# Kernel tuning notes

Hardware: AMD Instinct MI355X
Metric: run time of the kernel (lower is better)

The kernel has to match this reference:

```python
import jax, jax.numpy as jnp
import numpy as np

B, NQ, C = 2, 10000, 256
M, L, K = 8, 3, 4
D = C // M
LEVEL_SHAPES = [(100, 100), (50, 50), (25, 25)]


def setup_inputs() -> dict:
    key = jax.random.key(0)
    ks = jax.random.split(key, 16)
    inp = {
        "query": jax.random.normal(ks[0], (B, NQ, C), jnp.float32),
        "reference_points": jax.random.uniform(ks[1], (B, NQ, 2), jnp.float32),
        "value0": jax.random.normal(ks[2], (B, C) + LEVEL_SHAPES[0], jnp.float32),
        "value1": jax.random.normal(ks[3], (B, C) + LEVEL_SHAPES[1], jnp.float32),
        "value2": jax.random.normal(ks[4], (B, C) + LEVEL_SHAPES[2], jnp.float32),
        "Wv": jax.random.normal(ks[5], (C, C), jnp.float32) * 0.02,
        "bv": jnp.zeros((C,), jnp.float32),
        "Ws": jax.random.normal(ks[6], (M * L * K * 2, C), jnp.float32) * 0.05,
        "bs": jax.random.normal(ks[7], (M * L * K * 2,), jnp.float32),
        "Wa": jax.random.normal(ks[8], (M * L * K, C), jnp.float32) * 0.02,
        "ba": jnp.zeros((M * L * K,), jnp.float32),
        "Wo": jax.random.normal(ks[9], (C, C), jnp.float32) * 0.02,
        "bo": jnp.zeros((C,), jnp.float32),
    }
    return inp


def _bilinear_sample(vflat, px, py, H, W):
    """grid_sample bilinear, align_corners=False, padding_mode='zeros'.
    vflat: (B, M, H*W, D); px, py: (B, M, Q, K) pixel coords. -> (B, M, Q, K, D)
    """
    b, m, q, k = px.shape
    x0 = jnp.floor(px)
    y0 = jnp.floor(py)
    wx1 = px - x0  # frac weights (grad 1 w.r.t. px, matching grid_sample)
    wy1 = py - y0
    wx0 = 1.0 - wx1
    wy0 = 1.0 - wy1

    def gather(xi, yi):
        valid = ((xi >= 0) & (xi <= W - 1) & (yi >= 0) & (yi <= H - 1)).astype(vflat.dtype)
        xc = jnp.clip(xi, 0, W - 1).astype(jnp.int32)
        yc = jnp.clip(yi, 0, H - 1).astype(jnp.int32)
        idx = (yc * W + xc).reshape(b, m, q * k)
        g = jnp.take_along_axis(vflat, idx[..., None], axis=2)  # (B,M,QK,D)
        return g.reshape(b, m, q, k, -1) * valid[..., None]

    out = (gather(x0, y0) * (wx0 * wy0)[..., None]
           + gather(x0 + 1, y0) * (wx1 * wy0)[..., None]
           + gather(x0, y0 + 1) * (wx0 * wy1)[..., None]
           + gather(x0 + 1, y0 + 1) * (wx1 * wy1)[..., None])
    return out


def reference(query, reference_points, value0, value1, value2,
              Wv, bv, Ws, bs, Wa, ba, Wo, bo):
    bsz, nq, c = query.shape
    dt = query.dtype
    # sampling offsets and attention weights
    off = (query @ Ws.T + bs).reshape(bsz, nq, M, L, K, 2)
    attn = jax.nn.softmax((query @ Wa.T + ba).reshape(bsz, nq, M, L * K), axis=-1)
    attn = attn.reshape(bsz, nq, M, L, K)

    out = jnp.zeros((bsz, nq, M, D), dt)
    for li, v in enumerate([value0, value1, value2]):
        H, W = v.shape[2], v.shape[3]
        # conv1x1 value projection -> per-head maps (B, M, H*W, D)
        proj = jnp.einsum('bchw,oc->bohw', v, Wv) + bv[None, :, None, None]
        vflat = proj.reshape(bsz, M, D, H * W).transpose(0, 1, 3, 2)
        norm = jnp.asarray([W, H], dt)
        loc = reference_points[:, :, None, None, :] + off[:, :, :, li, :, :] / norm  # (B,Q,M,K,2)
        # grid = loc*2-1; pixel = (grid+1)*size/2 - 0.5 = loc*size - 0.5
        px = (loc[..., 0] * W - 0.5).transpose(0, 2, 1, 3)  # (B,M,Q,K)
        py = (loc[..., 1] * H - 0.5).transpose(0, 2, 1, 3)
        sampled = _bilinear_sample(vflat, px, py, H, W)  # (B,M,Q,K,D)
        out = out + jnp.einsum('bmqkd,bqmk->bqmd', sampled, attn[:, :, :, li, :])

    out = out.reshape(bsz, nq, c)
    return out @ Wo.T + bo
```

## Files before the change

### kernel.cpp

```cpp
#include <hip/hip_runtime.h>
#include <cstddef>

#define B_ 2
#define NQ_ 10000
#define C_ 256
#define M_ 8
#define L_ 3
#define K_ 4
#define D_ 32
#define P_ 13125

typedef unsigned short u16;
typedef __attribute__((ext_vector_type(8))) short short8;
typedef __attribute__((ext_vector_type(4))) float f32x4;

static __device__ __forceinline__ u16 f2bf(float f) {
    union { float f; unsigned u; } x; x.f = f;
    unsigned r = x.u + 0x7fffu + ((x.u >> 16) & 1u);
    return (u16)(r >> 16);
}
static __device__ __forceinline__ short8 cvt8(const float4& a, const float4& b) {
    short8 r;
    r[0] = (short)f2bf(a.x); r[1] = (short)f2bf(a.y);
    r[2] = (short)f2bf(a.z); r[3] = (short)f2bf(a.w);
    r[4] = (short)f2bf(b.x); r[5] = (short)f2bf(b.y);
    r[6] = (short)f2bf(b.z); r[7] = (short)f2bf(b.w);
    return r;
}

__global__ __launch_bounds__(256) void proj_fused(
    const float* __restrict__ v0, const float* __restrict__ v1,
    const float* __restrict__ v2,
    const float* __restrict__ Wv, const float* __restrict__ bv,
    u16* __restrict__ proj)
{
    __shared__ u16 As[64 * 264];
    __shared__ u16 Bs[64 * 264];

    const int bid = blockIdx.x;
    const int rlo = bid & 7;
    const int tmp = bid >> 3;
    const int panel = tmp & 3;
    const int rowTile = (tmp >> 2) * 8 + rlo;
    if (rowTile >= 414) return;

    const int b  = rowTile / 207;
    const int tl = rowTile % 207;
    int lvl, p0, HW, base;
    if (tl < 157)      { lvl = 0; p0 = tl * 64;         HW = 10000; base = 0; }
    else if (tl < 197) { lvl = 1; p0 = (tl - 157) * 64; HW = 2500;  base = 10000; }
    else               { lvl = 2; p0 = (tl - 197) * 64; HW = 625;   base = 12500; }
    const float* V = (lvl == 0 ? v0 : (lvl == 1 ? v1 : v2)) + (size_t)b * 256 * HW;

    const int t = threadIdx.x;
    const int px  = t & 63;
    const int pxg = min(p0 + px, HW - 1);
    const int ch0 = t >> 6;
    #pragma unroll
    for (int g = 0; g < 8; ++g) {
        float vv[8];
        #pragma unroll
        for (int j = 0; j < 8; ++j)
            vv[j] = V[(size_t)(ch0 + 4 * (8 * g + j)) * HW + pxg];
        #pragma unroll
        for (int j = 0; j < 8; ++j)
            As[px * 264 + ch0 + 4 * (8 * g + j)] = f2bf(vv[j]);
    }
    const int o0 = panel * 64;
    #pragma unroll
    for (int i = 0; i < 8; ++i) {
        int idx = i * 256 + t;
        int col = idx >> 5;
        int kc  = (idx & 31) * 8;
        const float* Br = Wv + (size_t)(o0 + col) * 256 + kc;
        float4 f0 = *reinterpret_cast<const float4*>(Br);
        float4 f1 = *reinterpret_cast<const float4*>(Br + 4);
        *reinterpret_cast<short8*>(&Bs[col * 264 + kc]) = cvt8(f0, f1);
    }
    __syncthreads();

    const int w  = t >> 6;
    const int l  = t & 63;
    const int lr = l & 15;
    const int kb = (l >> 4) * 8;
    const int arow = w * 16 + lr;

    f32x4 acc[4] = {};
    #pragma unroll
    for (int k0 = 0; k0 < 256; k0 += 32) {
        short8 a  = *reinterpret_cast<const short8*>(&As[arow * 264 + kb + k0]);
        short8 b0 = *reinterpret_cast<const short8*>(&Bs[(0 * 16 + lr) * 264 + kb + k0]);
        short8 b1 = *reinterpret_cast<const short8*>(&Bs[(1 * 16 + lr) * 264 + kb + k0]);
        short8 b2 = *reinterpret_cast<const short8*>(&Bs[(2 * 16 + lr) * 264 + kb + k0]);
        short8 b3 = *reinterpret_cast<const short8*>(&Bs[(3 * 16 + lr) * 264 + kb + k0]);
        acc[0] = __builtin_amdgcn_mfma_f32_16x16x32_bf16(a, b0, acc[0], 0, 0, 0);
        acc[1] = __builtin_amdgcn_mfma_f32_16x16x32_bf16(a, b1, acc[1], 0, 0, 0);
        acc[2] = __builtin_amdgcn_mfma_f32_16x16x32_bf16(a, b2, acc[2], 0, 0, 0);
        acc[3] = __builtin_amdgcn_mfma_f32_16x16x32_bf16(a, b3, acc[3], 0, 0, 0);
    }

    const int orow = (l >> 4) * 4;
    #pragma unroll
    for (int ct = 0; ct < 4; ++ct) {
        const int col = o0 + ct * 16 + lr;
        const float bsv = bv[col];
        #pragma unroll
        for (int r = 0; r < 4; ++r) {
            const int prow = w * 16 + orow + r;
            if (p0 + prow < HW)
                proj[((size_t)b * P_ + base + p0 + prow) * 256 + col] =
                    f2bf(acc[ct][r] + bsv);
        }
    }
}

template <bool AF32, typename OutT>
__global__ __launch_bounds__(256) void gemm_panel(
    const void* __restrict__ Av, int rows, int nRowTiles, int npanel,
    const float* __restrict__ B1f, const float* __restrict__ bias1, int N1,
    const float* __restrict__ B2f, const float* __restrict__ bias2, int Ntot,
    OutT* __restrict__ Cout)
{
    __shared__ u16 Bs[64 * 264];

    const int bid  = blockIdx.x;
    const int rlo  = bid & 7;
    const int tmp  = bid >> 3;
    const int panel = tmp % npanel;
    const int rowTile = (tmp / npanel) * 8 + rlo;
    if (rowTile >= nRowTiles) return;

    const int t  = threadIdx.x;
    const int w  = t >> 6;
    const int l  = t & 63;
    const int row0 = rowTile * 128 + w * 32;
    const int o0   = panel * 64;
    const int lr = l & 15;
    const int kb = (l >> 4) * 8;

    const int ra0 = min(row0 + lr,      rows - 1);
    const int ra1 = min(row0 + 16 + lr, rows - 1);

    short8 a0r[8], a1r[8];
    if constexpr (AF32) {
        const float* Af  = (const float*)Av;
        const float* Ap0 = Af + (size_t)ra0 * 256 + kb;
        const float* Ap1 = Af + (size_t)ra1 * 256 + kb;
        #pragma unroll
        for (int s = 0; s < 8; ++s) {
            float4 x0 = *reinterpret_cast<const float4*>(Ap0 + s * 32);
            float4 y0 = *reinterpret_cast<const float4*>(Ap0 + s * 32 + 4);
            float4 x1 = *reinterpret_cast<const float4*>(Ap1 + s * 32);
            float4 y1 = *reinterpret_cast<const float4*>(Ap1 + s * 32 + 4);
            a0r[s] = cvt8(x0, y0);
            a1r[s] = cvt8(x1, y1);
        }
    } else {
        const u16* Af  = (const u16*)Av;
        const u16* Ap0 = Af + (size_t)ra0 * 256 + kb;
        const u16* Ap1 = Af + (size_t)ra1 * 256 + kb;
        #pragma unroll
        for (int s = 0; s < 8; ++s) {
            a0r[s] = *reinterpret_cast<const short8*>(Ap0 + s * 32);
            a1r[s] = *reinterpret_cast<const short8*>(Ap1 + s * 32);
        }
    }

    #pragma unroll
    for (int i = 0; i < 8; ++i) {
        int idx = i * 256 + t;
        int col = idx >> 5;
        int kc  = (idx & 31) * 8;
        int colg = min(o0 + col, Ntot - 1);
        const float* Br = ((colg < N1) ? B1f + (size_t)colg * 256
                                       : B2f + (size_t)(colg - N1) * 256) + kc;
        float4 f0 = *reinterpret_cast<const float4*>(Br);
        float4 f1 = *reinterpret_cast<const float4*>(Br + 4);
        *reinterpret_cast<short8*>(&Bs[col * 264 + kc]) = cvt8(f0, f1);
    }
    __syncthreads();

    f32x4 acc[2][4] = {};

    #pragma unroll
    for (int s = 0; s < 8; ++s) {
        const int k0 = s * 32;
        short8 b0 = *reinterpret_cast<const short8*>(&Bs[(0 * 16 + lr) * 264 + kb + k0]);
        short8 b1 = *reinterpret_cast<const short8*>(&Bs[(1 * 16 + lr) * 264 + kb + k0]);
        short8 b2 = *reinterpret_cast<const short8*>(&Bs[(2 * 16 + lr) * 264 + kb + k0]);
        short8 b3 = *reinterpret_cast<const short8*>(&Bs[(3 * 16 + lr) * 264 + kb + k0]);
        acc[0][0] = __builtin_amdgcn_mfma_f32_16x16x32_bf16(a0r[s], b0, acc[0][0], 0, 0, 0);
        acc[0][1] = __builtin_amdgcn_mfma_f32_16x16x32_bf16(a0r[s], b1, acc[0][1], 0, 0, 0);
        acc[0][2] = __builtin_amdgcn_mfma_f32_16x16x32_bf16(a0r[s], b2, acc[0][2], 0, 0, 0);
        acc[0][3] = __builtin_amdgcn_mfma_f32_16x16x32_bf16(a0r[s], b3, acc[0][3], 0, 0, 0);
        acc[1][0] = __builtin_amdgcn_mfma_f32_16x16x32_bf16(a1r[s], b0, acc[1][0], 0, 0, 0);
        acc[1][1] = __builtin_amdgcn_mfma_f32_16x16x32_bf16(a1r[s], b1, acc[1][1], 0, 0, 0);
        acc[1][2] = __builtin_amdgcn_mfma_f32_16x16x32_bf16(a1r[s], b2, acc[1][2], 0, 0, 0);
        acc[1][3] = __builtin_amdgcn_mfma_f32_16x16x32_bf16(a1r[s], b3, acc[1][3], 0, 0, 0);
    }

    const int orow = (l >> 4) * 4;
    #pragma unroll
    for (int ct = 0; ct < 4; ++ct) {
        const int col = o0 + ct * 16 + lr;
        if (col >= Ntot) continue;
        const float bsv = (col < N1) ? bias1[col] : bias2[col - N1];
        #pragma unroll
        for (int rt = 0; rt < 2; ++rt) {
            #pragma unroll
            for (int r = 0; r < 4; ++r) {
                const int row = row0 + rt * 16 + orow + r;
                if (row < rows) {
                    float val = acc[rt][ct][r] + bsv;
                    if constexpr (sizeof(OutT) == 2)
                        Cout[(size_t)row * Ntot + col] = (OutT)f2bf(val);
                    else
                        Cout[(size_t)row * Ntot + col] = (OutT)val;
                }
            }
        }
    }
}

__global__ __launch_bounds__(256) void sample_kernel(
    const float* __restrict__ S,
    const float* __restrict__ refp,
    const u16* __restrict__ proj,
    u16* __restrict__ out2)
{
    constexpr int Wd[3]   = {100, 50, 25};
    constexpr int offs[3] = {0, 10000, 12500};

    __shared__ int   midx[192][4];
    __shared__ float mw[192][4];

    const int t = threadIdx.x;

    if (t < 192) {
        const int q  = t / 96;
        const int tq = t % 96;
        const int tm = tq / 12;
        const int tj = tq % 12;
        const int bq = blockIdx.x * 2 + q;
        const float* Sq = S + (size_t)bq * 288;

        float lg[12], mx = -1e30f;
        #pragma unroll
        for (int jj = 0; jj < 12; ++jj) {
            lg[jj] = Sq[192 + tm * 12 + jj];
            mx = fmaxf(mx, lg[jj]);
        }
        float sum = 0.f;
        #pragma unroll
        for (int jj = 0; jj < 12; ++jj) sum += __expf(lg[jj] - mx);
        const float attn = __expf(lg[tj] - mx) / sum;

        const int l  = tj >> 2;
        const int Wl = Wd[l];
        const float refx = refp[(size_t)bq * 2 + 0];
        const float refy = refp[(size_t)bq * 2 + 1];
        const float ox = Sq[(tm * 12 + tj) * 2 + 0];
        const float oy = Sq[(tm * 12 + tj) * 2 + 1];
        const float px = refx * (float)Wl + ox - 0.5f;
        const float py = refy * (float)Wl + oy - 0.5f;
        const float x0f = floorf(px), y0f = floorf(py);
        const float wx1 = px - x0f, wy1 = py - y0f;
        const float wx0 = 1.f - wx1, wy0 = 1.f - wy1;
        const int x0 = (int)x0f, y0 = (int)y0f;
        const int x1 = x0 + 1, y1 = y0 + 1;
        const bool vx0 = (unsigned)x0 < (unsigned)Wl;
        const bool vx1 = (unsigned)x1 < (unsigned)Wl;
        const bool vy0 = (unsigned)y0 < (unsigned)Wl;
        const bool vy1 = (unsigned)y1 < (unsigned)Wl;
        const int chb  = tm * 32;
        const int base = offs[l];
        midx[t][0] = (vx0 && vy0) ? ((base + y0 * Wl + x0) * 256 + chb) : 0;
        midx[t][1] = (vx1 && vy0) ? ((base + y0 * Wl + x1) * 256 + chb) : 0;
        midx[t][2] = (vx0 && vy1) ? ((base + y1 * Wl + x0) * 256 + chb) : 0;
        midx[t][3] = (vx1 && vy1) ? ((base + y1 * Wl + x1) * 256 + chb) : 0;
        mw[t][0] = (vx0 && vy0) ? attn * wx0 * wy0 : 0.f;
        mw[t][1] = (vx1 && vy0) ? attn * wx1 * wy0 : 0.f;
        mw[t][2] = (vx0 && vy1) ? attn * wx0 * wy1 : 0.f;
        mw[t][3] = (vx1 && vy1) ? attn * wx1 * wy1 : 0.f;
    }
    __syncthreads();

    const int qi  = t >> 7;
    const int tt  = t & 127;
    const int mh  = tt >> 4;
    const int d16 = tt & 15;
    const int bq2 = blockIdx.x * 2 + qi;
    const int b   = bq2 / NQ_;
    const u16* projb = proj + (size_t)b * P_ * 256 + 2 * d16;

    float acc0 = 0.f, acc1 = 0.f;

    #pragma unroll
    for (int j = 0; j < 12; ++j) {
        const int mj = qi * 96 + mh * 12 + j;
        const int4   o  = *reinterpret_cast<const int4*>(midx[mj]);
        const float4 ww = *reinterpret_cast<const float4*>(mw[mj]);
        const unsigned u00 = *reinterpret_cast<const unsigned*>(projb + o.x);
        const unsigned u10 = *reinterpret_cast<const unsigned*>(projb + o.y);
        const unsigned u01 = *reinterpret_cast<const unsigned*>(projb + o.z);
        const unsigned u11 = *reinterpret_cast<const unsigned*>(projb + o.w);
        union { unsigned u; float f; } c0, c1;
        c0.u = u00 << 16;          c1.u = u00 & 0xffff0000u;
        acc0 = fmaf(ww.x, c0.f, acc0); acc1 = fmaf(ww.x, c1.f, acc1);
        c0.u = u10 << 16;          c1.u = u10 & 0xffff0000u;
        acc0 = fmaf(ww.y, c0.f, acc0); acc1 = fmaf(ww.y, c1.f, acc1);
        c0.u = u01 << 16;          c1.u = u01 & 0xffff0000u;
        acc0 = fmaf(ww.z, c0.f, acc0); acc1 = fmaf(ww.z, c1.f, acc1);
        c0.u = u11 << 16;          c1.u = u11 & 0xffff0000u;
        acc0 = fmaf(ww.w, c0.f, acc0); acc1 = fmaf(ww.w, c1.f, acc1);
    }

    const unsigned packed = (unsigned)f2bf(acc0) | ((unsigned)f2bf(acc1) << 16);
    *reinterpret_cast<unsigned*>(out2 + (size_t)bq2 * 256 + mh * 32 + 2 * d16) = packed;
}

extern "C" void kernel_launch(void* const* d_in, const int* in_sizes, int n_in,
                              void* d_out, int out_size, void* d_ws, size_t ws_size,
                              hipStream_t stream)
{
    const float* query = (const float*)d_in[0];
    const float* refp  = (const float*)d_in[1];
    const float* v0    = (const float*)d_in[2];
    const float* v1    = (const float*)d_in[3];
    const float* v2    = (const float*)d_in[4];
    const float* Wv    = (const float*)d_in[5];
    const float* bv    = (const float*)d_in[6];
    const float* Ws    = (const float*)d_in[7];
    const float* bs    = (const float*)d_in[8];
    const float* Wa    = (const float*)d_in[9];
    const float* ba    = (const float*)d_in[10];
    const float* Wo    = (const float*)d_in[11];
    const float* bo    = (const float*)d_in[12];
    float* out = (float*)d_out;

    char* wsb = (char*)d_ws;
    u16*   proj = (u16*)wsb;    wsb += (size_t)B_ * P_ * 256 * 2;
    float* S    = (float*)wsb;  wsb += (size_t)B_ * NQ_ * 288 * 4;
    u16*   out2 = (u16*)wsb;    wsb += (size_t)B_ * NQ_ * 256 * 2;

    dim3 blk(256);

    proj_fused<<<dim3(1664), blk, 0, stream>>>(v0, v1, v2, Wv, bv, proj);

    gemm_panel<true, float><<<dim3(800), blk, 0, stream>>>(
        query, B_ * NQ_, 157, 5, Ws, bs, 192, Wa, ba, 288, S);

    sample_kernel<<<dim3(NQ_), blk, 0, stream>>>(S, refp, proj, out2);

    gemm_panel<false, float><<<dim3(640), blk, 0, stream>>>(
        out2, B_ * NQ_, 157, 4, Wo, bo, 256, Wo, bo, 256, out);
}
```

Baseline: 206.1 us.

## Store offsets/logits in bf16 and widen sampling gathers to 4 channels per thread

The offset/attention GEMM now writes its 288-wide output S in bf16 rather than fp32, which halves that intermediate's write and read traffic. The sampling kernel now handles 4 queries per block instead of 2, and each thread gathers 8-byte chunks (4 channels) per bilinear corner instead of 4 bytes, so it issues fewer and wider loads. Precomputation of the 384 sample entries loops across threads. Storing sampling offsets in bf16 loses precision in pixel coordinates, which could affect accuracy.

```diff
diff --git a/kernel.cpp b/kernel.cpp
--- a/kernel.cpp
+++ b/kernel.cpp
@@ -18,6 +18,10 @@
     union { float f; unsigned u; } x; x.f = f;
     unsigned r = x.u + 0x7fffu + ((x.u >> 16) & 1u);
     return (u16)(r >> 16);
+}
+static __device__ __forceinline__ float bf2f(u16 u) {
+    union { unsigned u; float f; } x; x.u = (unsigned)u << 16;
+    return x.f;
 }
 static __device__ __forceinline__ short8 cvt8(const float4& a, const float4& b) {
     short8 r;
@@ -223,7 +227,7 @@
 }
 
 __global__ __launch_bounds__(256) void sample_kernel(
-    const float* __restrict__ S,
+    const u16* __restrict__ S,
     const float* __restrict__ refp,
     const u16* __restrict__ proj,
     u16* __restrict__ out2)
@@ -231,23 +235,23 @@
     constexpr int Wd[3]   = {100, 50, 25};
     constexpr int offs[3] = {0, 10000, 12500};
 
-    __shared__ int   midx[192][4];
-    __shared__ float mw[192][4];
+    __shared__ int   midx[384][4];
+    __shared__ float mw[384][4];
 
     const int t = threadIdx.x;
 
-    if (t < 192) {
-        const int q  = t / 96;
-        const int tq = t % 96;
+    for (int e = t; e < 384; e += 256) {
+        const int q  = e / 96;
+        const int tq = e % 96;
         const int tm = tq / 12;
         const int tj = tq % 12;
-        const int bq = blockIdx.x * 2 + q;
-        const float* Sq = S + (size_t)bq * 288;
+        const int bq = blockIdx.x * 4 + q;
+        const u16* Sq = S + (size_t)bq * 288;
 
         float lg[12], mx = -1e30f;
         #pragma unroll
         for (int jj = 0; jj < 12; ++jj) {
-            lg[jj] = Sq[192 + tm * 12 + jj];
+            lg[jj] = bf2f(Sq[192 + tm * 12 + jj]);
             mx = fmaxf(mx, lg[jj]);
         }
         float sum = 0.f;
@@ -259,8 +263,8 @@
         const int Wl = Wd[l];
         const float refx = refp[(size_t)bq * 2 + 0];
         const float refy = refp[(size_t)bq * 2 + 1];
-        const float ox = Sq[(tm * 12 + tj) * 2 + 0];
-        const float oy = Sq[(tm * 12 + tj) * 2 + 1];
+        const float ox = bf2f(Sq[(tm * 12 + tj) * 2 + 0]);
+        const float oy = bf2f(Sq[(tm * 12 + tj) * 2 + 1]);
         const float px = refx * (float)Wl + ox - 0.5f;
         const float py = refy * (float)Wl + oy - 0.5f;
         const float x0f = floorf(px), y0f = floorf(py);
@@ -274,49 +278,52 @@
         const bool vy1 = (unsigned)y1 < (unsigned)Wl;
         const int chb  = tm * 32;
         const int base = offs[l];
-        midx[t][0] = (vx0 && vy0) ? ((base + y0 * Wl + x0) * 256 + chb) : 0;
-        midx[t][1] = (vx1 && vy0) ? ((base + y0 * Wl + x1) * 256 + chb) : 0;
-        midx[t][2] = (vx0 && vy1) ? ((base + y1 * Wl + x0) * 256 + chb) : 0;
-        midx[t][3] = (vx1 && vy1) ? ((base + y1 * Wl + x1) * 256 + chb) : 0;
-        mw[t][0] = (vx0 && vy0) ? attn * wx0 * wy0 : 0.f;
-        mw[t][1] = (vx1 && vy0) ? attn * wx1 * wy0 : 0.f;
-        mw[t][2] = (vx0 && vy1) ? attn * wx0 * wy1 : 0.f;
-        mw[t][3] = (vx1 && vy1) ? attn * wx1 * wy1 : 0.f;
+        midx[e][0] = (vx0 && vy0) ? ((base + y0 * Wl + x0) * 256 + chb) : 0;
+        midx[e][1] = (vx1 && vy0) ? ((base + y0 * Wl + x1) * 256 + chb) : 0;
+        midx[e][2] = (vx0 && vy1) ? ((base + y1 * Wl + x0) * 256 + chb) : 0;
+        midx[e][3] = (vx1 && vy1) ? ((base + y1 * Wl + x1) * 256 + chb) : 0;
+        mw[e][0] = (vx0 && vy0) ? attn * wx0 * wy0 : 0.f;
+        mw[e][1] = (vx1 && vy0) ? attn * wx1 * wy0 : 0.f;
+        mw[e][2] = (vx0 && vy1) ? attn * wx0 * wy1 : 0.f;
+        mw[e][3] = (vx1 && vy1) ? attn * wx1 * wy1 : 0.f;
     }
     __syncthreads();
 
-    const int qi  = t >> 7;
-    const int tt  = t & 127;
-    const int mh  = tt >> 4;
-    const int d16 = tt & 15;
-    const int bq2 = blockIdx.x * 2 + qi;
+    const int qi  = t >> 6;
+    const int r   = t & 63;
+    const int mh  = r >> 3;
+    const int d8  = r & 7;
+    const int bq2 = blockIdx.x * 4 + qi;
     const int b   = bq2 / NQ_;
-    const u16* projb = proj + (size_t)b * P_ * 256 + 2 * d16;
-
-    float acc0 = 0.f, acc1 = 0.f;
+    const u16* projb = proj + (size_t)b * P_ * 256 + 4 * d8;
+
+    float a0 = 0.f, a1 = 0.f, a2 = 0.f, a3 = 0.f;
 
     #pragma unroll
     for (int j = 0; j < 12; ++j) {
         const int mj = qi * 96 + mh * 12 + j;
         const int4   o  = *reinterpret_cast<const int4*>(midx[mj]);
         const float4 ww = *reinterpret_cast<const float4*>(mw[mj]);
-        const unsigned u00 = *reinterpret_cast<const unsigned*>(projb + o.x);
-        const unsigned u10 = *reinterpret_cast<const unsigned*>(projb + o.y);
-        const unsigned u01 = *reinterpret_cast<const unsigned*>(projb + o.z);
-        const unsigned u11 = *reinterpret_cast<const unsigned*>(projb + o.w);
-        union { unsigned u; float f; } c0, c1;
-        c0.u = u00 << 16;          c1.u = u00 & 0xffff0000u;
-        acc0 = fmaf(ww.x, c0.f, acc0); acc1 = fmaf(ww.x, c1.f, acc1);
-        c0.u = u10 << 16;          c1.u = u10 & 0xffff0000u;
-        acc0 = fmaf(ww.y, c0.f, acc0); acc1 = fmaf(ww.y, c1.f, acc1);
-        c0.u = u01 << 16;          c1.u = u01 & 0xffff0000u;
-        acc0 = fmaf(ww.z, c0.f, acc0); acc1 = fmaf(ww.z, c1.f, acc1);
-        c0.u = u11 << 16;          c1.u = u11 & 0xffff0000u;
-        acc0 = fmaf(ww.w, c0.f, acc0); acc1 = fmaf(ww.w, c1.f, acc1);
-    }
-
-    const unsigned packed = (unsigned)f2bf(acc0) | ((unsigned)f2bf(acc1) << 16);
-    *reinterpret_cast<unsigned*>(out2 + (size_t)bq2 * 256 + mh * 32 + 2 * d16) = packed;
+        const int* op = &o.x;
+        const float* wp = &ww.x;
+        #pragma unroll
+        for (int c = 0; c < 4; ++c) {
+            const uint2 u = *reinterpret_cast<const uint2*>(projb + op[c]);
+            const float wgt = wp[c];
+            union { unsigned q; float f; } e0, e1, e2, e3;
+            e0.q = u.x << 16; e1.q = u.x & 0xffff0000u;
+            e2.q = u.y << 16; e3.q = u.y & 0xffff0000u;
+            a0 = fmaf(wgt, e0.f, a0);
+            a1 = fmaf(wgt, e1.f, a1);
+            a2 = fmaf(wgt, e2.f, a2);
+            a3 = fmaf(wgt, e3.f, a3);
+        }
+    }
+
+    uint2 p;
+    p.x = (unsigned)f2bf(a0) | ((unsigned)f2bf(a1) << 16);
+    p.y = (unsigned)f2bf(a2) | ((unsigned)f2bf(a3) << 16);
+    *reinterpret_cast<uint2*>(out2 + (size_t)bq2 * 256 + mh * 32 + 4 * d8) = p;
 }
 
 extern "C" void kernel_launch(void* const* d_in, const int* in_sizes, int n_in,
@@ -340,17 +347,17 @@
 
     char* wsb = (char*)d_ws;
     u16*   proj = (u16*)wsb;    wsb += (size_t)B_ * P_ * 256 * 2;
-    float* S    = (float*)wsb;  wsb += (size_t)B_ * NQ_ * 288 * 4;
+    u16*   S    = (u16*)wsb;    wsb += (size_t)B_ * NQ_ * 288 * 2;
     u16*   out2 = (u16*)wsb;    wsb += (size_t)B_ * NQ_ * 256 * 2;
 
     dim3 blk(256);
 
     proj_fused<<<dim3(1664), blk, 0, stream>>>(v0, v1, v2, Wv, bv, proj);
 
-    gemm_panel<true, float><<<dim3(800), blk, 0, stream>>>(
+    gemm_panel<true, u16><<<dim3(800), blk, 0, stream>>>(
         query, B_ * NQ_, 157, 5, Ws, bs, 192, Wa, ba, 288, S);
 
-    sample_kernel<<<dim3(NQ_), blk, 0, stream>>>(S, refp, proj, out2);
+    sample_kernel<<<dim3(NQ_ * B_ / 4), blk, 0, stream>>>(S, refp, proj, out2);
 
     gemm_panel<false, float><<<dim3(640), blk, 0, stream>>>(
         out2, B_ * NQ_, 157, 4, Wo, bo, 256, Wo, bo, 256, out);
```

Result: slower. 211.5 us (+2.6%).

## Loop output panels in proj kernel, enlarge GEMM row tiles, pre-convert query to bf16

Applied to the files above, without the earlier changes.

The value projection kernel now handles one 64-pixel row tile per block and loops over all four output panels. The transposed value gather and bf16 conversion are done once instead of four times, and the A fragments stay in registers. The query/output GEMMs use 256-row tiles with 4 fragments per wave, which halves the number of B-panel loads from weights. The fp32 query is converted to bf16 in a separate pass first. This adds a launch and extra traffic, uses more registers, and leaves fewer blocks (414, 395, 316) to fill the GPU.

```diff
diff --git a/kernel.cpp b/kernel.cpp
--- a/kernel.cpp
+++ b/kernel.cpp
@@ -28,6 +28,16 @@
     return r;
 }
 
+__global__ __launch_bounds__(256) void cvt_q(
+    const float* __restrict__ src, u16* __restrict__ dst)
+{
+    const int i4 = (blockIdx.x * 256 + threadIdx.x) * 4;
+    float4 v = *reinterpret_cast<const float4*>(src + i4);
+    ushort4 o;
+    o.x = f2bf(v.x); o.y = f2bf(v.y); o.z = f2bf(v.z); o.w = f2bf(v.w);
+    *reinterpret_cast<ushort4*>(dst + i4) = o;
+}
+
 __global__ __launch_bounds__(256) void proj_fused(
     const float* __restrict__ v0, const float* __restrict__ v1,
     const float* __restrict__ v2,
@@ -37,20 +47,17 @@
     __shared__ u16 As[64 * 264];
     __shared__ u16 Bs[64 * 264];
 
-    const int bid = blockIdx.x;
-    const int rlo = bid & 7;
-    const int tmp = bid >> 3;
-    const int panel = tmp & 3;
-    const int rowTile = (tmp >> 2) * 8 + rlo;
-    if (rowTile >= 414) return;
-
+    const int rowTile = blockIdx.x;
     const int b  = rowTile / 207;
     const int tl = rowTile % 207;
-    int lvl, p0, HW, base;
-    if (tl < 157)      { lvl = 0; p0 = tl * 64;         HW = 10000; base = 0; }
-    else if (tl < 197) { lvl = 1; p0 = (tl - 157) * 64; HW = 2500;  base = 10000; }
-    else               { lvl = 2; p0 = (tl - 197) * 64; HW = 625;   base = 12500; }
-    const float* V = (lvl == 0 ? v0 : (lvl == 1 ? v1 : v2)) + (size_t)b * 256 * HW;
+    int p0, HW, base;
+    const float* V;
+    if (tl < 157)      { p0 = tl * 64;         HW = 10000; base = 0;
+                         V = v0 + (size_t)b * 256 * 10000; }
+    else if (tl < 197) { p0 = (tl - 157) * 64; HW = 2500;  base = 10000;
+                         V = v1 + (size_t)b * 256 * 2500; }
+    else               { p0 = (tl - 197) * 64; HW = 625;   base = 12500;
+                         V = v2 + (size_t)b * 256 * 625; }
 
     const int t = threadIdx.x;
     const int px  = t & 63;
@@ -65,17 +72,6 @@
         #pragma unroll
         for (int j = 0; j < 8; ++j)
             As[px * 264 + ch0 + 4 * (8 * g + j)] = f2bf(vv[j]);
-    }
-    const int o0 = panel * 64;
-    #pragma unroll
-    for (int i = 0; i < 8; ++i) {
-        int idx = i * 256 + t;
-        int col = idx >> 5;
-        int kc  = (idx & 31) * 8;
-        const float* Br = Wv + (size_t)(o0 + col) * 256 + kc;
-        float4 f0 = *reinterpret_cast<const float4*>(Br);
-        float4 f1 = *reinterpret_cast<const float4*>(Br + 4);
-        *reinterpret_cast<short8*>(&Bs[col * 264 + kc]) = cvt8(f0, f1);
     }
     __syncthreads();
 
@@ -85,85 +81,83 @@
     const int kb = (l >> 4) * 8;
     const int arow = w * 16 + lr;
 
-    f32x4 acc[4] = {};
-    #pragma unroll
-    for (int k0 = 0; k0 < 256; k0 += 32) {
-        short8 a  = *reinterpret_cast<const short8*>(&As[arow * 264 + kb + k0]);
-        short8 b0 = *reinterpret_cast<const short8*>(&Bs[(0 * 16 + lr) * 264 + kb + k0]);
-        short8 b1 = *reinterpret_cast<const short8*>(&Bs[(1 * 16 + lr) * 264 + kb + k0]);
-        short8 b2 = *reinterpret_cast<const short8*>(&Bs[(2 * 16 + lr) * 264 + kb + k0]);
-        short8 b3 = *reinterpret_cast<const short8*>(&Bs[(3 * 16 + lr) * 264 + kb + k0]);
-        acc[0] = __builtin_amdgcn_mfma_f32_16x16x32_bf16(a, b0, acc[0], 0, 0, 0);
-        acc[1] = __builtin_amdgcn_mfma_f32_16x16x32_bf16(a, b1, acc[1], 0, 0, 0);
-        acc[2] = __builtin_amdgcn_mfma_f32_16x16x32_bf16(a, b2, acc[2], 0, 0, 0);
-        acc[3] = __builtin_amdgcn_mfma_f32_16x16x32_bf16(a, b3, acc[3], 0, 0, 0);
-    }
-
-    const int orow = (l >> 4) * 4;
-    #pragma unroll
-    for (int ct = 0; ct < 4; ++ct) {
-        const int col = o0 + ct * 16 + lr;
-        const float bsv = bv[col];
-        #pragma unroll
-        for (int r = 0; r < 4; ++r) {
-            const int prow = w * 16 + orow + r;
-            if (p0 + prow < HW)
-                proj[((size_t)b * P_ + base + p0 + prow) * 256 + col] =
-                    f2bf(acc[ct][r] + bsv);
-        }
-    }
-}
-
-template <bool AF32, typename OutT>
-__global__ __launch_bounds__(256) void gemm_panel(
-    const void* __restrict__ Av, int rows, int nRowTiles, int npanel,
+    short8 a[8];
+    #pragma unroll
+    for (int s = 0; s < 8; ++s)
+        a[s] = *reinterpret_cast<const short8*>(&As[arow * 264 + kb + s * 32]);
+
+    for (int p = 0; p < 4; ++p) {
+        __syncthreads();
+        const int o0 = p * 64;
+        #pragma unroll
+        for (int i = 0; i < 8; ++i) {
+            int idx = i * 256 + t;
+            int col = idx >> 5;
+            int kc  = (idx & 31) * 8;
+            const float* Br = Wv + (size_t)(o0 + col) * 256 + kc;
+            float4 f0 = *reinterpret_cast<const float4*>(Br);
+            float4 f1 = *reinterpret_cast<const float4*>(Br + 4);
+            *reinterpret_cast<short8*>(&Bs[col * 264 + kc]) = cvt8(f0, f1);
+        }
+        __syncthreads();
+
+        f32x4 acc[4] = {};
+        #pragma unroll
+        for (int s = 0; s < 8; ++s) {
+            const int k0 = s * 32;
+            short8 b0 = *reinterpret_cast<const short8*>(&Bs[(0 * 16 + lr) * 264 + kb + k0]);
+            short8 b1 = *reinterpret_cast<const short8*>(&Bs[(1 * 16 + lr) * 264 + kb + k0]);
+            short8 b2 = *reinterpret_cast<const short8*>(&Bs[(2 * 16 + lr) * 264 + kb + k0]);
+            short8 b3 = *reinterpret_cast<const short8*>(&Bs[(3 * 16 + lr) * 264 + kb + k0]);
+            acc[0] = __builtin_amdgcn_mfma_f32_16x16x32_bf16(a[s], b0, acc[0], 0, 0, 0);
+            acc[1] = __builtin_amdgcn_mfma_f32_16x16x32_bf16(a[s], b1, acc[1], 0, 0, 0);
+            acc[2] = __builtin_amdgcn_mfma_f32_16x16x32_bf16(a[s], b2, acc[2], 0, 0, 0);
+            acc[3] = __builtin_amdgcn_mfma_f32_16x16x32_bf16(a[s], b3, acc[3], 0, 0, 0);
+        }
+
+        const int orow = (l >> 4) * 4;
+        #pragma unroll
+        for (int ct = 0; ct < 4; ++ct) {
+            const int col = o0 + ct * 16 + lr;
+            const float bsv = bv[col];
+            #pragma unroll
+            for (int r = 0; r < 4; ++r) {
+                const int prow = w * 16 + orow + r;
+                if (p0 + prow < HW)
+                    proj[((size_t)b * P_ + base + p0 + prow) * 256 + col] =
+                        f2bf(acc[ct][r] + bsv);
+            }
+        }
+    }
+}
+
+template <typename OutT>
+__global__ __launch_bounds__(256) void gemm_reg(
+    const u16* __restrict__ A, int rows, int npanel,
     const float* __restrict__ B1f, const float* __restrict__ bias1, int N1,
     const float* __restrict__ B2f, const float* __restrict__ bias2, int Ntot,
     OutT* __restrict__ Cout)
 {
     __shared__ u16 Bs[64 * 264];
 
-    const int bid  = blockIdx.x;
-    const int rlo  = bid & 7;
-    const int tmp  = bid >> 3;
-    const int panel = tmp % npanel;
-    const int rowTile = (tmp / npanel) * 8 + rlo;
-    if (rowTile >= nRowTiles) return;
-
+    const int rowTile = blockIdx.x / npanel;
+    const int panel   = blockIdx.x % npanel;
     const int t  = threadIdx.x;
     const int w  = t >> 6;
     const int l  = t & 63;
-    const int row0 = rowTile * 128 + w * 32;
-    const int o0   = panel * 64;
     const int lr = l & 15;
     const int kb = (l >> 4) * 8;
-
-    const int ra0 = min(row0 + lr,      rows - 1);
-    const int ra1 = min(row0 + 16 + lr, rows - 1);
-
-    short8 a0r[8], a1r[8];
-    if constexpr (AF32) {
-        const float* Af  = (const float*)Av;
-        const float* Ap0 = Af + (size_t)ra0 * 256 + kb;
-        const float* Ap1 = Af + (size_t)ra1 * 256 + kb;
-        #pragma unroll
-        for (int s = 0; s < 8; ++s) {
-            float4 x0 = *reinterpret_cast<const float4*>(Ap0 + s * 32);
-            float4 y0 = *reinterpret_cast<const float4*>(Ap0 + s * 32 + 4);
-            float4 x1 = *reinterpret_cast<const float4*>(Ap1 + s * 32);
-            float4 y1 = *reinterpret_cast<const float4*>(Ap1 + s * 32 + 4);
-            a0r[s] = cvt8(x0, y0);
-            a1r[s] = cvt8(x1, y1);
-        }
-    } else {
-        const u16* Af  = (const u16*)Av;
-        const u16* Ap0 = Af + (size_t)ra0 * 256 + kb;
-        const u16* Ap1 = Af + (size_t)ra1 * 256 + kb;
-        #pragma unroll
-        for (int s = 0; s < 8; ++s) {
-            a0r[s] = *reinterpret_cast<const short8*>(Ap0 + s * 32);
-            a1r[s] = *reinterpret_cast<const short8*>(Ap1 + s * 32);
-        }
+    const int o0 = panel * 64;
+    const int rbase = rowTile * 256 + w * 64;
+
+    short8 a[4][8];
+    #pragma unroll
+    for (int f = 0; f < 4; ++f) {
+        const int ra = min(rbase + f * 16 + lr, rows - 1);
+        const u16* Ap = A + (size_t)ra * 256 + kb;
+        #pragma unroll
+        for (int s = 0; s < 8; ++s)
+            a[f][s] = *reinterpret_cast<const short8*>(Ap + s * 32);
     }
 
     #pragma unroll
@@ -180,7 +174,7 @@
     }
     __syncthreads();
 
-    f32x4 acc[2][4] = {};
+    f32x4 acc[4][4] = {};
 
     #pragma unroll
     for (int s = 0; s < 8; ++s) {
@@ -189,14 +183,13 @@
         short8 b1 = *reinterpret_cast<const short8*>(&Bs[(1 * 16 + lr) * 264 + kb + k0]);
         short8 b2 = *reinterpret_cast<const short8*>(&Bs[(2 * 16 + lr) * 264 + kb + k0]);
         short8 b3 = *reinterpret_cast<const short8*>(&Bs[(3 * 16 + lr) * 264 + kb + k0]);
-        acc[0][0] = __builtin_amdgcn_mfma_f32_16x16x32_bf16(a0r[s], b0, acc[0][0], 0, 0, 0);
-        acc[0][1] = __builtin_amdgcn_mfma_f32_16x16x32_bf16(a0r[s], b1, acc[0][1], 0, 0, 0);
-        acc[0][2] = __builtin_amdgcn_mfma_f32_16x16x32_bf16(a0r[s], b2, acc[0][2], 0, 0, 0);
-        acc[0][3] = __builtin_amdgcn_mfma_f32_16x16x32_bf16(a0r[s], b3, acc[0][3], 0, 0, 0);
-        acc[1][0] = __builtin_amdgcn_mfma_f32_16x16x32_bf16(a1r[s], b0, acc[1][0], 0, 0, 0);
-        acc[1][1] = __builtin_amdgcn_mfma_f32_16x16x32_bf16(a1r[s], b1, acc[1][1], 0, 0, 0);
-        acc[1][2] = __builtin_amdgcn_mfma_f32_16x16x32_bf16(a1r[s], b2, acc[1][2], 0, 0, 0);
-        acc[1][3] = __builtin_amdgcn_mfma_f32_16x16x32_bf16(a1r[s], b3, acc[1][3], 0, 0, 0);
+        #pragma unroll
+        for (int f = 0; f < 4; ++f) {
+            acc[f][0] = __builtin_amdgcn_mfma_f32_16x16x32_bf16(a[f][s], b0, acc[f][0], 0, 0, 0);
+            acc[f][1] = __builtin_amdgcn_mfma_f32_16x16x32_bf16(a[f][s], b1, acc[f][1], 0, 0, 0);
+            acc[f][2] = __builtin_amdgcn_mfma_f32_16x16x32_bf16(a[f][s], b2, acc[f][2], 0, 0, 0);
+            acc[f][3] = __builtin_amdgcn_mfma_f32_16x16x32_bf16(a[f][s], b3, acc[f][3], 0, 0, 0);
+        }
     }
 
     const int orow = (l >> 4) * 4;
@@ -206,12 +199,12 @@
         if (col >= Ntot) continue;
         const float bsv = (col < N1) ? bias1[col] : bias2[col - N1];
         #pragma unroll
-        for (int rt = 0; rt < 2; ++rt) {
+        for (int f = 0; f < 4; ++f) {
             #pragma unroll
             for (int r = 0; r < 4; ++r) {
-                const int row = row0 + rt * 16 + orow + r;
+                const int row = rbase + f * 16 + orow + r;
                 if (row < rows) {
-                    float val = acc[rt][ct][r] + bsv;
+                    float val = acc[f][ct][r] + bsv;
                     if constexpr (sizeof(OutT) == 2)
                         Cout[(size_t)row * Ntot + col] = (OutT)f2bf(val);
                     else
@@ -342,16 +335,19 @@
     u16*   proj = (u16*)wsb;    wsb += (size_t)B_ * P_ * 256 * 2;
     float* S    = (float*)wsb;  wsb += (size_t)B_ * NQ_ * 288 * 4;
     u16*   out2 = (u16*)wsb;    wsb += (size_t)B_ * NQ_ * 256 * 2;
+    u16*   qbf  = (u16*)wsb;    wsb += (size_t)B_ * NQ_ * 256 * 2;
 
     dim3 blk(256);
 
-    proj_fused<<<dim3(1664), blk, 0, stream>>>(v0, v1, v2, Wv, bv, proj);
-
-    gemm_panel<true, float><<<dim3(800), blk, 0, stream>>>(
-        query, B_ * NQ_, 157, 5, Ws, bs, 192, Wa, ba, 288, S);
+    cvt_q<<<dim3(5000), blk, 0, stream>>>(query, qbf);
+
+    proj_fused<<<dim3(414), blk, 0, stream>>>(v0, v1, v2, Wv, bv, proj);
+
+    gemm_reg<float><<<dim3(79 * 5), blk, 0, stream>>>(
+        qbf, B_ * NQ_, 5, Ws, bs, 192, Wa, ba, 288, S);
 
     sample_kernel<<<dim3(NQ_), blk, 0, stream>>>(S, refp, proj, out2);
 
-    gemm_panel<false, float><<<dim3(640), blk, 0, stream>>>(
-        out2, B_ * NQ_, 157, 4, Wo, bo, 256, Wo, bo, 256, out);
-}
+    gemm_reg<float><<<dim3(79 * 4), blk, 0, stream>>>(
+        out2, B_ * NQ_, 4, Wo, bo, 256, Wo, bo, 256, out);
+}
```

Measured after the change: 206.1 us. About the same (-0.0%).
